# Performance work log

Measured on AMD Instinct MI355X. Metric: run time of the kernel, lower is better.

The kernel has to match this reference:

```python
import jax, jax.numpy as jnp
import numpy as np

D_MODEL = 1024
NUM_HEADS = 16
D_FF = 4096
B = 4
S = 1024
EPS = 1e-5


def _dense_params(key, fan_in, fan_out):
    kw, kb = jax.random.split(key)
    lim = (6.0 / (fan_in + fan_out)) ** 0.5
    w = jax.random.uniform(kw, (fan_in, fan_out), jnp.float32, -lim, lim)
    b = jnp.zeros((fan_out,), jnp.float32)
    return w, b


def setup_inputs() -> dict:
    key = jax.random.key(0)
    ks = jax.random.split(key, 20)
    inp = {
        "x": jax.random.normal(ks[0], (B, S, D_MODEL), jnp.float32),
        "enc_outputs": jax.random.normal(ks[1], (B, S, D_MODEL), jnp.float32),
        "dec_pad_mask": jnp.zeros((B, 1, S, S), jnp.float32),
        "dec_subseq_mask": jnp.zeros((B, 1, S, S), jnp.float32),
    }
    # MHA1 params
    for i, name in enumerate(["wq1", "wk1", "wv1", "wo1"]):
        w, b = _dense_params(ks[2 + i], D_MODEL, D_MODEL)
        inp[name + "_w"], inp[name + "_b"] = w, b
    # MHA2 params
    for i, name in enumerate(["wq2", "wk2", "wv2", "wo2"]):
        w, b = _dense_params(ks[6 + i], D_MODEL, D_MODEL)
        inp[name + "_w"], inp[name + "_b"] = w, b
    # FFN params
    inp["ffn1_w"], inp["ffn1_b"] = _dense_params(ks[10], D_MODEL, D_FF)
    inp["ffn2_w"], inp["ffn2_b"] = _dense_params(ks[11], D_FF, D_MODEL)
    # LayerNorm params
    for i in (1, 2, 3):
        inp[f"ln{i}_g"] = jnp.ones((D_MODEL,), jnp.float32)
        inp[f"ln{i}_b"] = jnp.zeros((D_MODEL,), jnp.float32)
    return inp


def _layernorm(x, g, b):
    mu = jnp.mean(x, axis=-1, keepdims=True)
    var = jnp.mean(jnp.square(x - mu), axis=-1, keepdims=True)
    return (x - mu) * jax.lax.rsqrt(var + EPS) * g + b


def _mha(q_in, k_in, v_in, mask, wq_w, wq_b, wk_w, wk_b, wv_w, wv_b, wo_w, wo_b):
    Bq, Sq, D = q_in.shape
    Sk = k_in.shape[1]
    H = NUM_HEADS
    d = D // H
    # project then split heads: (B, H, S, d)
    q = (q_in @ wq_w + wq_b).reshape(Bq, Sq, H, d).transpose(0, 2, 1, 3)
    k = (k_in @ wk_w + wk_b).reshape(Bq, Sk, H, d).transpose(0, 2, 1, 3)
    v = (v_in @ wv_w + wv_b).reshape(Bq, Sk, H, d).transpose(0, 2, 1, 3)
    logits = jnp.einsum("bhqd,bhkd->bhqk", q, k) / jnp.sqrt(jnp.float32(d))
    if mask is not None:
        logits = logits + mask[:, :, :, :logits.shape[-1]]
    weights = jax.nn.softmax(logits, axis=-1)  # (B, H, Sq, Sk)
    attn = jnp.einsum("bhqk,bhkd->bhqd", weights, v)
    attn = attn.transpose(0, 2, 1, 3).reshape(Bq, Sq, D)
    out = attn @ wo_w + wo_b
    return out, weights


def reference(x, enc_outputs, dec_pad_mask, dec_subseq_mask,
              wq1_w, wq1_b, wk1_w, wk1_b, wv1_w, wv1_b, wo1_w, wo1_b,
              wq2_w, wq2_b, wk2_w, wk2_b, wv2_w, wv2_b, wo2_w, wo2_b,
              ffn1_w, ffn1_b, ffn2_w, ffn2_b,
              ln1_g, ln1_b, ln2_g, ln2_b, ln3_g, ln3_b):
    # self-attention (dropout is identity at inference)
    mha1, attn_w1 = _mha(x, x, x, dec_subseq_mask,
                         wq1_w, wq1_b, wk1_w, wk1_b, wv1_w, wv1_b, wo1_w, wo1_b)
    out1 = _layernorm(mha1 + x, ln1_g, ln1_b)
    # cross-attention
    mha2, attn_w2 = _mha(out1, enc_outputs, enc_outputs, dec_pad_mask,
                         wq2_w, wq2_b, wk2_w, wk2_b, wv2_w, wv2_b, wo2_w, wo2_b)
    out2 = _layernorm(mha2 + out1, ln2_g, ln2_b)
    # FFN
    ffn = jax.nn.relu(out2 @ ffn1_w + ffn1_b) @ ffn2_w + ffn2_b
    out3 = _layernorm(ffn + out2, ln3_g, ln3_b)
    return out3, attn_w1, attn_w2
```

## Files before the change

kernel.cpp:

```cpp
#include <hip/hip_runtime.h>

typedef unsigned short u16;
typedef unsigned int u32;
typedef unsigned long long u64;
typedef __bf16 bf16x8 __attribute__((ext_vector_type(8)));
typedef float f32x4 __attribute__((ext_vector_type(4)));

#define AS1 __attribute__((address_space(1)))
#define AS3 __attribute__((address_space(3)))

__device__ __forceinline__ float bf2f(u32 v) {
    u32 u = v << 16;
    float f;
    __builtin_memcpy(&f, &u, 4);
    return f;
}
__device__ __forceinline__ u16 f2bf(float f) {
    u32 u;
    __builtin_memcpy(&u, &f, 4);
    u32 r = u + 0x7FFFu + ((u >> 16) & 1u);
    return (u16)(r >> 16);
}

template <int BM, int BN, bool RELU, bool SCORES, bool AF32>
__global__ __launch_bounds__(256) void gemm_bt(
    const void* __restrict__ Av, const u16* __restrict__ Bt,
    const float* __restrict__ bias, void* __restrict__ Cv,
    int lda, int ldb, int ldc, int K,
    long Aob, long Aoh, long Bob, long Boh, long Cob, long Coh,
    int batchH, const float* __restrict__ mask, float scale)
{
    const int tid = threadIdx.x;
    const int z = blockIdx.z;
    const int bb = z / batchH, hh = z % batchH;
    const u16*   A16 = AF32 ? nullptr : ((const u16*)Av + (size_t)bb * Aob + (size_t)hh * Aoh);
    const float* A32 = AF32 ? ((const float*)Av + (size_t)bb * Aob + (size_t)hh * Aoh) : nullptr;
    Bt += (size_t)bb * Bob + (size_t)hh * Boh;
    u16*   C16 = SCORES ? nullptr : ((u16*)Cv + (size_t)bb * Cob + (size_t)hh * Coh);
    float* C32 = SCORES ? ((float*)Cv + (size_t)bb * Cob + (size_t)hh * Coh) : nullptr;
    const float* maskp = SCORES ? (mask + ((size_t)bb << 20)) : nullptr;

    const int m0 = blockIdx.y * BM;
    const int n0 = blockIdx.x * BN;

    __shared__ bf16x8 As[AF32 ? BM * 8 : BM * 4];
    __shared__ bf16x8 Bs[BN * 4];

    constexpr int TM = (BN == 128) ? 4 : 2;
    constexpr int TN = 4;
    const int wave = tid >> 6, lane = tid & 63;
    const int wr = (BN == 128) ? (wave >> 1) : wave;
    const int wc = (BN == 128) ? (wave & 1) : 0;
    const int row_base = wr * (TM * 16);
    const int col_base = wc * 64;
    const int quad = lane >> 4, l16 = lane & 15;

    f32x4 acc[TM][TN] = {};

    for (int k0 = 0; k0 < K; k0 += 32) {
        if (AF32) {
#pragma unroll
            for (int i = 0; i < (BM * 8) / 256; ++i) {
                int s = tid + i * 256;
                int row = s >> 3;
                int gq = (s & 7) ^ (row & 7);
                const float* gp = A32 + (size_t)(m0 + row) * lda + k0 + gq * 4;
                __builtin_amdgcn_global_load_lds((AS1 const void*)gp, (AS3 void*)&As[s], 16, 0, 0);
            }
        } else {
#pragma unroll
            for (int i = 0; i < (BM * 4) / 256; ++i) {
                int s = tid + i * 256;
                int row = s >> 2;
                int gq = (s & 3) ^ ((s >> 3) & 3);
                const u16* gp = A16 + (size_t)(m0 + row) * lda + k0 + gq * 8;
                __builtin_amdgcn_global_load_lds((AS1 const void*)gp, (AS3 void*)&As[s], 16, 0, 0);
            }
        }
#pragma unroll
        for (int i = 0; i < (BN * 4) / 256; ++i) {
            int s = tid + i * 256;
            int row = s >> 2;
            int gq = (s & 3) ^ ((s >> 3) & 3);
            const u16* gp = Bt + (size_t)(n0 + row) * ldb + k0 + gq * 8;
            __builtin_amdgcn_global_load_lds((AS1 const void*)gp, (AS3 void*)&Bs[s], 16, 0, 0);
        }
        __syncthreads();

        bf16x8 af[TM], bfr[TN];
#pragma unroll
        for (int ri = 0; ri < TM; ++ri) {
            int r = row_base + ri * 16 + l16;
            if (AF32) {
                const f32x4* Asf = (const f32x4*)As;
                int rx = r & 7;
                f32x4 a0 = Asf[r * 8 + ((2 * quad) ^ rx)];
                f32x4 a1 = Asf[r * 8 + ((2 * quad + 1) ^ rx)];
                union { bf16x8 v; u16 u[8]; } cc;
                cc.u[0] = f2bf(a0[0]); cc.u[1] = f2bf(a0[1]);
                cc.u[2] = f2bf(a0[2]); cc.u[3] = f2bf(a0[3]);
                cc.u[4] = f2bf(a1[0]); cc.u[5] = f2bf(a1[1]);
                cc.u[6] = f2bf(a1[2]); cc.u[7] = f2bf(a1[3]);
                af[ri] = cc.v;
            } else {
                af[ri] = As[r * 4 + (quad ^ ((r >> 1) & 3))];
            }
        }
#pragma unroll
        for (int cj = 0; cj < TN; ++cj) {
            int c = col_base + cj * 16 + l16;
            bfr[cj] = Bs[c * 4 + (quad ^ ((c >> 1) & 3))];
        }
#pragma unroll
        for (int ri = 0; ri < TM; ++ri)
#pragma unroll
            for (int cj = 0; cj < TN; ++cj)
                acc[ri][cj] = __builtin_amdgcn_mfma_f32_16x16x32_bf16(af[ri], bfr[cj], acc[ri][cj], 0, 0, 0);
        __syncthreads();
    }

#pragma unroll
    for (int ri = 0; ri < TM; ++ri) {
#pragma unroll
        for (int cj = 0; cj < TN; ++cj) {
            const int col = n0 + col_base + cj * 16 + l16;
            const float bv = (!SCORES && bias) ? bias[col] : 0.0f;
#pragma unroll
            for (int r = 0; r < 4; ++r) {
                const int row = m0 + row_base + ri * 16 + quad * 4 + r;
                float v = acc[ri][cj][r];
                if (SCORES) {
                    C32[(size_t)row * ldc + col] = v * scale + maskp[((size_t)row << 10) + col];
                } else {
                    v += bv;
                    if (RELU) v = fmaxf(v, 0.0f);
                    C16[(size_t)row * ldc + col] = f2bf(v);
                }
            }
        }
    }
}

__global__ void transpose_cvt(const float* __restrict__ src, u16* __restrict__ dst, int R, int C)
{
    __shared__ u16 t[32][33];
    const int c0 = blockIdx.x << 5, r0 = blockIdx.y << 5;
    const int tx = threadIdx.x, ty = threadIdx.y;
#pragma unroll
    for (int i = 0; i < 4; ++i) {
        int r = r0 + ty * 4 + i;
        t[ty * 4 + i][tx] = f2bf(src[(size_t)r * C + c0 + tx]);
    }
    __syncthreads();
#pragma unroll
    for (int i = 0; i < 4; ++i) {
        int c = c0 + ty * 4 + i;
        dst[(size_t)c * R + r0 + tx] = t[tx][ty * 4 + i];
    }
}

__global__ __launch_bounds__(256) void cvt4(const float* __restrict__ src, u16* __restrict__ dst)
{
    size_t i = (size_t)blockIdx.x * 256 + threadIdx.x;
    f32x4 v = ((const f32x4*)src)[i];
    u64 o = (u64)f2bf(v[0]) | ((u64)f2bf(v[1]) << 16) | ((u64)f2bf(v[2]) << 32) | ((u64)f2bf(v[3]) << 48);
    ((u64*)dst)[i] = o;
}

__global__ void transpose_v(const u16* __restrict__ v, u16* __restrict__ vt)
{
    __shared__ u16 t[32][33];
    const int z = blockIdx.z, b = z >> 4, h = z & 15;
    const int s0 = blockIdx.x << 5, d0 = blockIdx.y << 5;
    const int tx = threadIdx.x, ty = threadIdx.y;
    const u16* src = v + ((size_t)b << 20) + h * 64;
#pragma unroll
    for (int i = 0; i < 4; ++i) {
        int s = s0 + ty * 4 + i;
        t[ty * 4 + i][tx] = src[((size_t)s << 10) + d0 + tx];
    }
    __syncthreads();
    u16* dst = vt + ((size_t)z << 16);
#pragma unroll
    for (int i = 0; i < 4; ++i) {
        int d = d0 + ty * 4 + i;
        dst[((size_t)d << 10) + s0 + tx] = t[tx][ty * 4 + i];
    }
}

__global__ __launch_bounds__(256) void softmax_rows_f32(float* __restrict__ data)
{
    float* p = data + ((size_t)blockIdx.x << 10);
    const int t = threadIdx.x;
    f32x4 v = ((const f32x4*)p)[t];
    float mx = fmaxf(fmaxf(v[0], v[1]), fmaxf(v[2], v[3]));
#pragma unroll
    for (int off = 32; off > 0; off >>= 1) mx = fmaxf(mx, __shfl_xor(mx, off));
    __shared__ float sred[4];
    const int wave = t >> 6, lane = t & 63;
    if (lane == 0) sred[wave] = mx;
    __syncthreads();
    mx = fmaxf(fmaxf(sred[0], sred[1]), fmaxf(sred[2], sred[3]));
    __syncthreads();
    float e0 = __expf(v[0] - mx), e1 = __expf(v[1] - mx);
    float e2 = __expf(v[2] - mx), e3 = __expf(v[3] - mx);
    float s = e0 + e1 + e2 + e3;
#pragma unroll
    for (int off = 32; off > 0; off >>= 1) s += __shfl_xor(s, off);
    if (lane == 0) sred[wave] = s;
    __syncthreads();
    const float inv = 1.0f / (sred[0] + sred[1] + sred[2] + sred[3]);
    f32x4 o;
    o[0] = e0 * inv; o[1] = e1 * inv; o[2] = e2 * inv; o[3] = e3 * inv;
    ((f32x4*)p)[t] = o;
}

template <bool B_F32>
__global__ __launch_bounds__(256) void add_ln(
    const u16* __restrict__ a, const void* __restrict__ bvp,
    const float* __restrict__ g, const float* __restrict__ be,
    u16* __restrict__ out, float* __restrict__ outf)
{
    const size_t row = blockIdx.x;
    const int t = threadIdx.x;
    uint2 va = ((const uint2*)(a + (row << 10)))[t];
    float f0 = bf2f(va.x & 0xffffu), f1 = bf2f(va.x >> 16);
    float f2 = bf2f(va.y & 0xffffu), f3 = bf2f(va.y >> 16);
    if (B_F32) {
        f32x4 vb = ((const f32x4*)((const float*)bvp + (row << 10)))[t];
        f0 += vb[0]; f1 += vb[1]; f2 += vb[2]; f3 += vb[3];
    } else {
        uint2 vb = ((const uint2*)((const u16*)bvp + (row << 10)))[t];
        f0 += bf2f(vb.x & 0xffffu); f1 += bf2f(vb.x >> 16);
        f2 += bf2f(vb.y & 0xffffu); f3 += bf2f(vb.y >> 16);
    }
    float s = f0 + f1 + f2 + f3;
    float q = f0 * f0 + f1 * f1 + f2 * f2 + f3 * f3;
#pragma unroll
    for (int off = 32; off > 0; off >>= 1) {
        s += __shfl_xor(s, off);
        q += __shfl_xor(q, off);
    }
    __shared__ float rs[4], rq[4];
    const int wave = t >> 6, lane = t & 63;
    if (lane == 0) { rs[wave] = s; rq[wave] = q; }
    __syncthreads();
    s = rs[0] + rs[1] + rs[2] + rs[3];
    q = rq[0] + rq[1] + rq[2] + rq[3];
    const float mean = s * (1.0f / 1024.0f);
    const float var = q * (1.0f / 1024.0f) - mean * mean;
    const float rstd = rsqrtf(var + 1e-5f);
    f32x4 vg = ((const f32x4*)g)[t];
    f32x4 ve = ((const f32x4*)be)[t];
    float r0 = (f0 - mean) * rstd * vg[0] + ve[0];
    float r1 = (f1 - mean) * rstd * vg[1] + ve[1];
    float r2 = (f2 - mean) * rstd * vg[2] + ve[2];
    float r3 = (f3 - mean) * rstd * vg[3] + ve[3];
    if (out) {
        u32 o0 = (u32)f2bf(r0) | ((u32)f2bf(r1) << 16);
        u32 o1 = (u32)f2bf(r2) | ((u32)f2bf(r3) << 16);
        ((uint2*)(out + (row << 10)))[t] = make_uint2(o0, o1);
    }
    if (outf) {
        f32x4 o; o[0] = r0; o[1] = r1; o[2] = r2; o[3] = r3;
        ((f32x4*)(outf + (row << 10)))[t] = o;
    }
}

extern "C" void kernel_launch(void* const* d_in, const int* in_sizes, int n_in,
                              void* d_out, int out_size, void* d_ws, size_t ws_size,
                              hipStream_t stream)
{
    const float* X    = (const float*)d_in[0];
    const float* ENC  = (const float*)d_in[1];
    const float* MPAD = (const float*)d_in[2];
    const float* MSUB = (const float*)d_in[3];
    const float* Wq1 = (const float*)d_in[4],  *bq1 = (const float*)d_in[5];
    const float* Wk1 = (const float*)d_in[6],  *bk1 = (const float*)d_in[7];
    const float* Wv1 = (const float*)d_in[8],  *bv1 = (const float*)d_in[9];
    const float* Wo1 = (const float*)d_in[10], *bo1 = (const float*)d_in[11];
    const float* Wq2 = (const float*)d_in[12], *bq2 = (const float*)d_in[13];
    const float* Wk2 = (const float*)d_in[14], *bk2 = (const float*)d_in[15];
    const float* Wv2 = (const float*)d_in[16], *bv2 = (const float*)d_in[17];
    const float* Wo2 = (const float*)d_in[18], *bo2 = (const float*)d_in[19];
    const float* Wf1 = (const float*)d_in[20], *bf1 = (const float*)d_in[21];
    const float* Wf2 = (const float*)d_in[22], *bf2v = (const float*)d_in[23];
    const float* g1 = (const float*)d_in[24], *be1 = (const float*)d_in[25];
    const float* g2 = (const float*)d_in[26], *be2 = (const float*)d_in[27];
    const float* g3 = (const float*)d_in[28], *be3 = (const float*)d_in[29];

    float* OUT3 = (float*)d_out;
    float* AW1  = OUT3 + 4194304;
    float* AW2  = AW1 + 67108864;

    u16* ws = (u16*)d_ws;
    const size_t M1 = 1048576;
    u16* WTq1 = ws + 0 * M1, *WTk1 = ws + 1 * M1, *WTv1 = ws + 2 * M1, *WTo1 = ws + 3 * M1;
    u16* WTq2 = ws + 4 * M1, *WTk2 = ws + 5 * M1, *WTv2 = ws + 6 * M1, *WTo2 = ws + 7 * M1;
    u16* WTF1 = ws + 8 * M1;
    u16* WTF2 = ws + 12 * M1;
    u16* Xbf  = ws + 16 * M1;
    u16* ENCb = ws + 20 * M1;
    u16* Qb = ws + 24 * M1, *Kb = ws + 28 * M1, *Vb = ws + 32 * M1, *VT = ws + 36 * M1;
    u16* Hb = Qb;
    u16* ATT = ws + 40 * M1, *TMP = ws + 44 * M1, *O1 = ws + 48 * M1, *O2 = ws + 52 * M1;

    const dim3 tb(32, 8);
    cvt4<<<4096, 256, 0, stream>>>(X, Xbf);
    cvt4<<<4096, 256, 0, stream>>>(ENC, ENCb);
    transpose_cvt<<<dim3(32, 32), tb, 0, stream>>>(Wq1, WTq1, 1024, 1024);
    transpose_cvt<<<dim3(32, 32), tb, 0, stream>>>(Wk1, WTk1, 1024, 1024);
    transpose_cvt<<<dim3(32, 32), tb, 0, stream>>>(Wv1, WTv1, 1024, 1024);
    transpose_cvt<<<dim3(32, 32), tb, 0, stream>>>(Wo1, WTo1, 1024, 1024);
    transpose_cvt<<<dim3(32, 32), tb, 0, stream>>>(Wq2, WTq2, 1024, 1024);
    transpose_cvt<<<dim3(32, 32), tb, 0, stream>>>(Wk2, WTk2, 1024, 1024);
    transpose_cvt<<<dim3(32, 32), tb, 0, stream>>>(Wv2, WTv2, 1024, 1024);
    transpose_cvt<<<dim3(32, 32), tb, 0, stream>>>(Wo2, WTo2, 1024, 1024);
    transpose_cvt<<<dim3(128, 32), tb, 0, stream>>>(Wf1, WTF1, 1024, 4096);
    transpose_cvt<<<dim3(32, 128), tb, 0, stream>>>(Wf2, WTF2, 4096, 1024);

    gemm_bt<128, 128, false, false, false><<<dim3(8, 32, 1), 256, 0, stream>>>(
        Xbf, WTq1, bq1, Qb, 1024, 1024, 1024, 1024, 0, 0, 0, 0, 0, 0, 1, nullptr, 0.f);
    gemm_bt<128, 128, false, false, false><<<dim3(8, 32, 1), 256, 0, stream>>>(
        Xbf, WTk1, bk1, Kb, 1024, 1024, 1024, 1024, 0, 0, 0, 0, 0, 0, 1, nullptr, 0.f);
    gemm_bt<128, 128, false, false, false><<<dim3(8, 32, 1), 256, 0, stream>>>(
        Xbf, WTv1, bv1, Vb, 1024, 1024, 1024, 1024, 0, 0, 0, 0, 0, 0, 1, nullptr, 0.f);
    transpose_v<<<dim3(32, 2, 64), tb, 0, stream>>>(Vb, VT);
    gemm_bt<128, 128, false, true, false><<<dim3(8, 8, 64), 256, 0, stream>>>(
        Qb, Kb, nullptr, AW1, 1024, 1024, 1024, 64,
        1048576, 64, 1048576, 64, 16777216, 1048576, 16, MSUB, 0.125f);
    softmax_rows_f32<<<65536, 256, 0, stream>>>(AW1);
    gemm_bt<128, 64, false, false, true><<<dim3(1, 8, 64), 256, 0, stream>>>(
        AW1, VT, nullptr, ATT, 1024, 1024, 1024, 1024,
        16777216, 1048576, 1048576, 65536, 1048576, 64, 16, nullptr, 0.f);
    gemm_bt<128, 128, false, false, false><<<dim3(8, 32, 1), 256, 0, stream>>>(
        ATT, WTo1, bo1, TMP, 1024, 1024, 1024, 1024, 0, 0, 0, 0, 0, 0, 1, nullptr, 0.f);
    add_ln<true><<<4096, 256, 0, stream>>>(TMP, X, g1, be1, O1, nullptr);

    gemm_bt<128, 128, false, false, false><<<dim3(8, 32, 1), 256, 0, stream>>>(
        O1, WTq2, bq2, Qb, 1024, 1024, 1024, 1024, 0, 0, 0, 0, 0, 0, 1, nullptr, 0.f);
    gemm_bt<128, 128, false, false, false><<<dim3(8, 32, 1), 256, 0, stream>>>(
        ENCb, WTk2, bk2, Kb, 1024, 1024, 1024, 1024, 0, 0, 0, 0, 0, 0, 1, nullptr, 0.f);
    gemm_bt<128, 128, false, false, false><<<dim3(8, 32, 1), 256, 0, stream>>>(
        ENCb, WTv2, bv2, Vb, 1024, 1024, 1024, 1024, 0, 0, 0, 0, 0, 0, 1, nullptr, 0.f);
    transpose_v<<<dim3(32, 2, 64), tb, 0, stream>>>(Vb, VT);
    gemm_bt<128, 128, false, true, false><<<dim3(8, 8, 64), 256, 0, stream>>>(
        Qb, Kb, nullptr, AW2, 1024, 1024, 1024, 64,
        1048576, 64, 1048576, 64, 16777216, 1048576, 16, MPAD, 0.125f);
    softmax_rows_f32<<<65536, 256, 0, stream>>>(AW2);
    gemm_bt<128, 64, false, false, true><<<dim3(1, 8, 64), 256, 0, stream>>>(
        AW2, VT, nullptr, ATT, 1024, 1024, 1024, 1024,
        16777216, 1048576, 1048576, 65536, 1048576, 64, 16, nullptr, 0.f);
    gemm_bt<128, 128, false, false, false><<<dim3(8, 32, 1), 256, 0, stream>>>(
        ATT, WTo2, bo2, TMP, 1024, 1024, 1024, 1024, 0, 0, 0, 0, 0, 0, 1, nullptr, 0.f);
    add_ln<false><<<4096, 256, 0, stream>>>(TMP, O1, g2, be2, O2, nullptr);

    gemm_bt<128, 128, true, false, false><<<dim3(32, 32, 1), 256, 0, stream>>>(
        O2, WTF1, bf1, Hb, 1024, 1024, 4096, 1024, 0, 0, 0, 0, 0, 0, 1, nullptr, 0.f);
    gemm_bt<128, 128, false, false, false><<<dim3(8, 32, 1), 256, 0, stream>>>(
        Hb, WTF2, bf2v, TMP, 4096, 4096, 1024, 4096, 0, 0, 0, 0, 0, 0, 1, nullptr, 0.f);
    add_ln<false><<<4096, 256, 0, stream>>>(TMP, O2, g3, be3, nullptr, OUT3);
}
```

Measured before the change: 1.523 ms.

## Fuse attention scores, softmax and PV into one kernel; merge QKV projections

Replaces the separate scores GEMM, row softmax, and f32-A PV GEMM with a fused two-pass attention kernel. The first pass computes the running row max and sum; the second recomputes scores, writes the normalized weights once, and multiplies by V from LDS. Q/K/V projections (and cross-attention K/V) are merged into single wider GEMMs with concatenated weights and biases, and the output projections use narrower tiles for more blocks. This removes the fp32 score round-trips through global memory, at the cost of computing QK^T twice.

```diff
diff --git a/kernel.cpp b/kernel.cpp
--- a/kernel.cpp
+++ b/kernel.cpp
@@ -22,28 +22,17 @@
     return (u16)(r >> 16);
 }
 
-template <int BM, int BN, bool RELU, bool SCORES, bool AF32>
+template <int BM, int BN, bool RELU>
 __global__ __launch_bounds__(256) void gemm_bt(
-    const void* __restrict__ Av, const u16* __restrict__ Bt,
-    const float* __restrict__ bias, void* __restrict__ Cv,
-    int lda, int ldb, int ldc, int K,
-    long Aob, long Aoh, long Bob, long Boh, long Cob, long Coh,
-    int batchH, const float* __restrict__ mask, float scale)
+    const u16* __restrict__ A, const u16* __restrict__ Bt,
+    const float* __restrict__ bias, u16* __restrict__ C,
+    int lda, int ldb, int ldc, int K)
 {
     const int tid = threadIdx.x;
-    const int z = blockIdx.z;
-    const int bb = z / batchH, hh = z % batchH;
-    const u16*   A16 = AF32 ? nullptr : ((const u16*)Av + (size_t)bb * Aob + (size_t)hh * Aoh);
-    const float* A32 = AF32 ? ((const float*)Av + (size_t)bb * Aob + (size_t)hh * Aoh) : nullptr;
-    Bt += (size_t)bb * Bob + (size_t)hh * Boh;
-    u16*   C16 = SCORES ? nullptr : ((u16*)Cv + (size_t)bb * Cob + (size_t)hh * Coh);
-    float* C32 = SCORES ? ((float*)Cv + (size_t)bb * Cob + (size_t)hh * Coh) : nullptr;
-    const float* maskp = SCORES ? (mask + ((size_t)bb << 20)) : nullptr;
-
     const int m0 = blockIdx.y * BM;
     const int n0 = blockIdx.x * BN;
 
-    __shared__ bf16x8 As[AF32 ? BM * 8 : BM * 4];
+    __shared__ bf16x8 As[BM * 4];
     __shared__ bf16x8 Bs[BN * 4];
 
     constexpr int TM = (BN == 128) ? 4 : 2;
@@ -58,24 +47,13 @@
     f32x4 acc[TM][TN] = {};
 
     for (int k0 = 0; k0 < K; k0 += 32) {
-        if (AF32) {
-#pragma unroll
-            for (int i = 0; i < (BM * 8) / 256; ++i) {
-                int s = tid + i * 256;
-                int row = s >> 3;
-                int gq = (s & 7) ^ (row & 7);
-                const float* gp = A32 + (size_t)(m0 + row) * lda + k0 + gq * 4;
-                __builtin_amdgcn_global_load_lds((AS1 const void*)gp, (AS3 void*)&As[s], 16, 0, 0);
-            }
-        } else {
-#pragma unroll
-            for (int i = 0; i < (BM * 4) / 256; ++i) {
-                int s = tid + i * 256;
-                int row = s >> 2;
-                int gq = (s & 3) ^ ((s >> 3) & 3);
-                const u16* gp = A16 + (size_t)(m0 + row) * lda + k0 + gq * 8;
-                __builtin_amdgcn_global_load_lds((AS1 const void*)gp, (AS3 void*)&As[s], 16, 0, 0);
-            }
+#pragma unroll
+        for (int i = 0; i < (BM * 4) / 256; ++i) {
+            int s = tid + i * 256;
+            int row = s >> 2;
+            int gq = (s & 3) ^ ((s >> 3) & 3);
+            const u16* gp = A + (size_t)(m0 + row) * lda + k0 + gq * 8;
+            __builtin_amdgcn_global_load_lds((AS1 const void*)gp, (AS3 void*)&As[s], 16, 0, 0);
         }
 #pragma unroll
         for (int i = 0; i < (BN * 4) / 256; ++i) {
@@ -91,20 +69,7 @@
 #pragma unroll
         for (int ri = 0; ri < TM; ++ri) {
             int r = row_base + ri * 16 + l16;
-            if (AF32) {
-                const f32x4* Asf = (const f32x4*)As;
-                int rx = r & 7;
-                f32x4 a0 = Asf[r * 8 + ((2 * quad) ^ rx)];
-                f32x4 a1 = Asf[r * 8 + ((2 * quad + 1) ^ rx)];
-                union { bf16x8 v; u16 u[8]; } cc;
-                cc.u[0] = f2bf(a0[0]); cc.u[1] = f2bf(a0[1]);
-                cc.u[2] = f2bf(a0[2]); cc.u[3] = f2bf(a0[3]);
-                cc.u[4] = f2bf(a1[0]); cc.u[5] = f2bf(a1[1]);
-                cc.u[6] = f2bf(a1[2]); cc.u[7] = f2bf(a1[3]);
-                af[ri] = cc.v;
-            } else {
-                af[ri] = As[r * 4 + (quad ^ ((r >> 1) & 3))];
-            }
+            af[ri] = As[r * 4 + (quad ^ ((r >> 1) & 3))];
         }
 #pragma unroll
         for (int cj = 0; cj < TN; ++cj) {
@@ -124,21 +89,190 @@
 #pragma unroll
         for (int cj = 0; cj < TN; ++cj) {
             const int col = n0 + col_base + cj * 16 + l16;
-            const float bv = (!SCORES && bias) ? bias[col] : 0.0f;
+            const float bv = bias ? bias[col] : 0.0f;
 #pragma unroll
             for (int r = 0; r < 4; ++r) {
                 const int row = m0 + row_base + ri * 16 + quad * 4 + r;
-                float v = acc[ri][cj][r];
-                if (SCORES) {
-                    C32[(size_t)row * ldc + col] = v * scale + maskp[((size_t)row << 10) + col];
-                } else {
-                    v += bv;
-                    if (RELU) v = fmaxf(v, 0.0f);
-                    C16[(size_t)row * ldc + col] = f2bf(v);
+                float v = acc[ri][cj][r] + bv;
+                if (RELU) v = fmaxf(v, 0.0f);
+                C[(size_t)row * ldc + col] = f2bf(v);
+            }
+        }
+    }
+}
+
+__global__ __launch_bounds__(256, 2) void attn_fused(
+    const u16* __restrict__ Qp, const u16* __restrict__ Kp, const u16* __restrict__ VTp,
+    const float* __restrict__ mask, float* __restrict__ AW, u16* __restrict__ ATT,
+    int ldq, int ldk)
+{
+    const int tid = threadIdx.x;
+    const int wave = tid >> 6, lane = tid & 63, quad = lane >> 4, l16 = lane & 15;
+    const int z = blockIdx.y, b = z >> 4, h = z & 15;
+    const int m0 = blockIdx.x << 7;
+
+    const u16* Q = Qp + (size_t)(b * 1024 + m0) * ldq + h * 64;
+    const u16* K = Kp + (size_t)(b * 1024) * ldk + h * 64;
+    const u16* VT = VTp + ((size_t)z << 16);
+    const float* Mq = mask + ((size_t)b << 20) + ((size_t)m0 << 10);
+    float* AWp = AW + ((size_t)z << 20) + ((size_t)m0 << 10);
+    u16* Op = ATT + ((size_t)(b * 1024 + m0) << 10) + h * 64;
+
+    __shared__ bf16x8 Qs[128 * 8];
+    __shared__ bf16x8 Ks[128 * 8];
+    __shared__ u64 Ps[4][1024];
+
+    bf16x8* Vs = Qs;
+
+#pragma unroll
+    for (int i = 0; i < 4; ++i) {
+        int s = tid + i * 256;
+        int row = s >> 3, ch = s & 7;
+        const u16* gp = Q + (size_t)row * ldq + ((ch ^ (row & 7)) << 3);
+        __builtin_amdgcn_global_load_lds((AS1 const void*)gp, (AS3 void*)&Qs[s], 16, 0, 0);
+    }
+    __syncthreads();
+
+    bf16x8 bq[2][2];
+#pragma unroll
+    for (int qj = 0; qj < 2; ++qj) {
+        int q = wave * 32 + qj * 16 + l16;
+#pragma unroll
+        for (int dstep = 0; dstep < 2; ++dstep)
+            bq[qj][dstep] = Qs[q * 8 + ((dstep * 4 + quad) ^ (q & 7))];
+    }
+
+    float m_run[2] = {-1e30f, -1e30f};
+    float l_run[2] = {0.0f, 0.0f};
+
+    for (int kt = 0; kt < 8; ++kt) {
+#pragma unroll
+        for (int i = 0; i < 4; ++i) {
+            int s = tid + i * 256;
+            int row = s >> 3, ch = s & 7;
+            const u16* gp = K + (size_t)(kt * 128 + row) * ldk + ((ch ^ (row & 7)) << 3);
+            __builtin_amdgcn_global_load_lds((AS1 const void*)gp, (AS3 void*)&Ks[s], 16, 0, 0);
+        }
+        __syncthreads();
+
+        f32x4 acc[8][2] = {};
+#pragma unroll
+        for (int ki = 0; ki < 8; ++ki) {
+            int key = ki * 16 + l16;
+            bf16x8 ka0 = Ks[key * 8 + (quad ^ (key & 7))];
+            bf16x8 ka1 = Ks[key * 8 + ((4 + quad) ^ (key & 7))];
+#pragma unroll
+            for (int qj = 0; qj < 2; ++qj) {
+                acc[ki][qj] = __builtin_amdgcn_mfma_f32_16x16x32_bf16(ka0, bq[qj][0], acc[ki][qj], 0, 0, 0);
+                acc[ki][qj] = __builtin_amdgcn_mfma_f32_16x16x32_bf16(ka1, bq[qj][1], acc[ki][qj], 0, 0, 0);
+            }
+        }
+#pragma unroll
+        for (int qj = 0; qj < 2; ++qj) {
+            const float* mrow = Mq + (((size_t)(wave * 32 + qj * 16 + l16)) << 10) + kt * 128 + quad * 4;
+            float mx = -1e30f;
+#pragma unroll
+            for (int ki = 0; ki < 8; ++ki) {
+                f32x4 mk = *(const f32x4*)(mrow + ki * 16);
+#pragma unroll
+                for (int r = 0; r < 4; ++r) {
+                    float s = fmaf(acc[ki][qj][r], 0.125f, mk[r]);
+                    acc[ki][qj][r] = s;
+                    mx = fmaxf(mx, s);
                 }
             }
-        }
-    }
+            mx = fmaxf(mx, __shfl_xor(mx, 16));
+            mx = fmaxf(mx, __shfl_xor(mx, 32));
+            float mnew = fmaxf(m_run[qj], mx);
+            float sum = 0.0f;
+#pragma unroll
+            for (int ki = 0; ki < 8; ++ki)
+#pragma unroll
+                for (int r = 0; r < 4; ++r)
+                    sum += __expf(acc[ki][qj][r] - mnew);
+            sum += __shfl_xor(sum, 16);
+            sum += __shfl_xor(sum, 32);
+            l_run[qj] = l_run[qj] * __expf(m_run[qj] - mnew) + sum;
+            m_run[qj] = mnew;
+        }
+        __syncthreads();
+    }
+
+    const float invl[2] = {1.0f / l_run[0], 1.0f / l_run[1]};
+    u64* Pw = Ps[wave];
+    const bf16x8* Pr = (const bf16x8*)Ps[wave];
+    f32x4 opv[4][2] = {};
+
+    for (int kt = 0; kt < 8; ++kt) {
+#pragma unroll
+        for (int i = 0; i < 4; ++i) {
+            int s = tid + i * 256;
+            int row = s >> 3, ch = s & 7;
+            const u16* gp = K + (size_t)(kt * 128 + row) * ldk + ((ch ^ (row & 7)) << 3);
+            __builtin_amdgcn_global_load_lds((AS1 const void*)gp, (AS3 void*)&Ks[s], 16, 0, 0);
+        }
+#pragma unroll
+        for (int i = 0; i < 4; ++i) {
+            int s = tid + i * 256;
+            int row = s >> 4, ch = s & 15;
+            const u16* gp = VT + ((size_t)row << 10) + kt * 128 + ((ch ^ (row & 15)) << 3);
+            __builtin_amdgcn_global_load_lds((AS1 const void*)gp, (AS3 void*)&Vs[s], 16, 0, 0);
+        }
+        __syncthreads();
+
+#pragma unroll
+        for (int ki = 0; ki < 8; ++ki) {
+            int key = ki * 16 + l16;
+            bf16x8 ka0 = Ks[key * 8 + (quad ^ (key & 7))];
+            bf16x8 ka1 = Ks[key * 8 + ((4 + quad) ^ (key & 7))];
+#pragma unroll
+            for (int qj = 0; qj < 2; ++qj) {
+                f32x4 a = {};
+                a = __builtin_amdgcn_mfma_f32_16x16x32_bf16(ka0, bq[qj][0], a, 0, 0, 0);
+                a = __builtin_amdgcn_mfma_f32_16x16x32_bf16(ka1, bq[qj][1], a, 0, 0, 0);
+                const size_t roff = ((size_t)(wave * 32 + qj * 16 + l16)) << 10;
+                f32x4 mk = *(const f32x4*)(Mq + roff + kt * 128 + ki * 16 + quad * 4);
+                f32x4 p;
+#pragma unroll
+                for (int r = 0; r < 4; ++r)
+                    p[r] = __expf(fmaf(a[r], 0.125f, mk[r]) - m_run[qj]) * invl[qj];
+                *(f32x4*)(AWp + roff + kt * 128 + ki * 16 + quad * 4) = p;
+                u64 pk = (u64)f2bf(p[0]) | ((u64)f2bf(p[1]) << 16)
+                       | ((u64)f2bf(p[2]) << 32) | ((u64)f2bf(p[3]) << 48);
+                int q = qj * 16 + l16;
+                Pw[q * 32 + ((ki * 4 + quad) ^ ((q & 7) << 1))] = pk;
+            }
+        }
+
+#pragma unroll
+        for (int ks = 0; ks < 4; ++ks) {
+            bf16x8 pb[2];
+#pragma unroll
+            for (int qj = 0; qj < 2; ++qj) {
+                int q = qj * 16 + l16;
+                pb[qj] = Pr[q * 16 + ((ks * 4 + quad) ^ (q & 7))];
+            }
+#pragma unroll
+            for (int ds = 0; ds < 4; ++ds) {
+                int d = ds * 16 + l16;
+                bf16x8 va = Vs[d * 16 + ((ks * 4 + quad) ^ (d & 15))];
+                opv[ds][0] = __builtin_amdgcn_mfma_f32_16x16x32_bf16(va, pb[0], opv[ds][0], 0, 0, 0);
+                opv[ds][1] = __builtin_amdgcn_mfma_f32_16x16x32_bf16(va, pb[1], opv[ds][1], 0, 0, 0);
+            }
+        }
+        __syncthreads();
+    }
+
+#pragma unroll
+    for (int ds = 0; ds < 4; ++ds)
+#pragma unroll
+        for (int qj = 0; qj < 2; ++qj) {
+            int q = wave * 32 + qj * 16 + l16;
+            f32x4 v = opv[ds][qj];
+            u64 o = (u64)f2bf(v[0]) | ((u64)f2bf(v[1]) << 16)
+                  | ((u64)f2bf(v[2]) << 32) | ((u64)f2bf(v[3]) << 48);
+            *(u64*)(Op + (((size_t)q) << 10) + ds * 16 + quad * 4) = o;
+        }
 }
 
 __global__ void transpose_cvt(const float* __restrict__ src, u16* __restrict__ dst, int R, int C)
@@ -167,17 +301,17 @@
     ((u64*)dst)[i] = o;
 }
 
-__global__ void transpose_v(const u16* __restrict__ v, u16* __restrict__ vt)
+__global__ void transpose_v(const u16* __restrict__ v, u16* __restrict__ vt, int ld)
 {
     __shared__ u16 t[32][33];
     const int z = blockIdx.z, b = z >> 4, h = z & 15;
     const int s0 = blockIdx.x << 5, d0 = blockIdx.y << 5;
     const int tx = threadIdx.x, ty = threadIdx.y;
-    const u16* src = v + ((size_t)b << 20) + h * 64;
+    const u16* src = v + (size_t)(b << 10) * ld + h * 64;
 #pragma unroll
     for (int i = 0; i < 4; ++i) {
         int s = s0 + ty * 4 + i;
-        t[ty * 4 + i][tx] = src[((size_t)s << 10) + d0 + tx];
+        t[ty * 4 + i][tx] = src[(size_t)s * ld + d0 + tx];
     }
     __syncthreads();
     u16* dst = vt + ((size_t)z << 16);
@@ -188,31 +322,12 @@
     }
 }
 
-__global__ __launch_bounds__(256) void softmax_rows_f32(float* __restrict__ data)
-{
-    float* p = data + ((size_t)blockIdx.x << 10);
-    const int t = threadIdx.x;
-    f32x4 v = ((const f32x4*)p)[t];
-    float mx = fmaxf(fmaxf(v[0], v[1]), fmaxf(v[2], v[3]));
-#pragma unroll
-    for (int off = 32; off > 0; off >>= 1) mx = fmaxf(mx, __shfl_xor(mx, off));
-    __shared__ float sred[4];
-    const int wave = t >> 6, lane = t & 63;
-    if (lane == 0) sred[wave] = mx;
-    __syncthreads();
-    mx = fmaxf(fmaxf(sred[0], sred[1]), fmaxf(sred[2], sred[3]));
-    __syncthreads();
-    float e0 = __expf(v[0] - mx), e1 = __expf(v[1] - mx);
-    float e2 = __expf(v[2] - mx), e3 = __expf(v[3] - mx);
-    float s = e0 + e1 + e2 + e3;
-#pragma unroll
-    for (int off = 32; off > 0; off >>= 1) s += __shfl_xor(s, off);
-    if (lane == 0) sred[wave] = s;
-    __syncthreads();
-    const float inv = 1.0f / (sred[0] + sred[1] + sred[2] + sred[3]);
-    f32x4 o;
-    o[0] = e0 * inv; o[1] = e1 * inv; o[2] = e2 * inv; o[3] = e3 * inv;
-    ((f32x4*)p)[t] = o;
+__global__ void concat3(const float* __restrict__ a, const float* __restrict__ b,
+                        const float* __restrict__ c, float* __restrict__ o, int n)
+{
+    int i = blockIdx.x * 256 + threadIdx.x;
+    float v = (i < n) ? a[i] : (i < 2 * n) ? b[i - n] : c[i - 2 * n];
+    o[i] = v;
 }
 
 template <bool B_F32>
@@ -295,69 +410,66 @@
 
     u16* ws = (u16*)d_ws;
     const size_t M1 = 1048576;
-    u16* WTq1 = ws + 0 * M1, *WTk1 = ws + 1 * M1, *WTv1 = ws + 2 * M1, *WTo1 = ws + 3 * M1;
-    u16* WTq2 = ws + 4 * M1, *WTk2 = ws + 5 * M1, *WTv2 = ws + 6 * M1, *WTo2 = ws + 7 * M1;
+    u16* WTqkv1 = ws + 0 * M1;
+    u16* WTo1 = ws + 3 * M1;
+    u16* WTkv2 = ws + 4 * M1;
+    u16* WTq2 = ws + 6 * M1;
+    u16* WTo2 = ws + 7 * M1;
     u16* WTF1 = ws + 8 * M1;
     u16* WTF2 = ws + 12 * M1;
     u16* Xbf  = ws + 16 * M1;
     u16* ENCb = ws + 20 * M1;
-    u16* Qb = ws + 24 * M1, *Kb = ws + 28 * M1, *Vb = ws + 32 * M1, *VT = ws + 36 * M1;
-    u16* Hb = Qb;
-    u16* ATT = ws + 40 * M1, *TMP = ws + 44 * M1, *O1 = ws + 48 * M1, *O2 = ws + 52 * M1;
+    u16* QKV1 = ws + 24 * M1;
+    u16* Q2b  = ws + 24 * M1;
+    u16* KV2  = ws + 28 * M1;
+    u16* Hb   = ws + 24 * M1;
+    u16* VT   = ws + 36 * M1;
+    u16* ATT  = ws + 40 * M1;
+    u16* TMP  = ws + 44 * M1;
+    u16* O1   = ws + 48 * M1;
+    u16* O2   = ws + 52 * M1;
+    float* BQKV1 = (float*)(ws + 56 * M1);
+    float* BKV2  = BQKV1 + 3072;
 
     const dim3 tb(32, 8);
     cvt4<<<4096, 256, 0, stream>>>(X, Xbf);
     cvt4<<<4096, 256, 0, stream>>>(ENC, ENCb);
-    transpose_cvt<<<dim3(32, 32), tb, 0, stream>>>(Wq1, WTq1, 1024, 1024);
-    transpose_cvt<<<dim3(32, 32), tb, 0, stream>>>(Wk1, WTk1, 1024, 1024);
-    transpose_cvt<<<dim3(32, 32), tb, 0, stream>>>(Wv1, WTv1, 1024, 1024);
+    transpose_cvt<<<dim3(32, 32), tb, 0, stream>>>(Wq1, WTqkv1, 1024, 1024);
+    transpose_cvt<<<dim3(32, 32), tb, 0, stream>>>(Wk1, WTqkv1 + 1 * M1, 1024, 1024);
+    transpose_cvt<<<dim3(32, 32), tb, 0, stream>>>(Wv1, WTqkv1 + 2 * M1, 1024, 1024);
     transpose_cvt<<<dim3(32, 32), tb, 0, stream>>>(Wo1, WTo1, 1024, 1024);
+    transpose_cvt<<<dim3(32, 32), tb, 0, stream>>>(Wk2, WTkv2, 1024, 1024);
+    transpose_cvt<<<dim3(32, 32), tb, 0, stream>>>(Wv2, WTkv2 + 1 * M1, 1024, 1024);
     transpose_cvt<<<dim3(32, 32), tb, 0, stream>>>(Wq2, WTq2, 1024, 1024);
-    transpose_cvt<<<dim3(32, 32), tb, 0, stream>>>(Wk2, WTk2, 1024, 1024);
-    transpose_cvt<<<dim3(32, 32), tb, 0, stream>>>(Wv2, WTv2, 1024, 1024);
     transpose_cvt<<<dim3(32, 32), tb, 0, stream>>>(Wo2, WTo2, 1024, 1024);
     transpose_cvt<<<dim3(128, 32), tb, 0, stream>>>(Wf1, WTF1, 1024, 4096);
     transpose_cvt<<<dim3(32, 128), tb, 0, stream>>>(Wf2, WTF2, 4096, 1024);
-
-    gemm_bt<128, 128, false, false, false><<<dim3(8, 32, 1), 256, 0, stream>>>(
-        Xbf, WTq1, bq1, Qb, 1024, 1024, 1024, 1024, 0, 0, 0, 0, 0, 0, 1, nullptr, 0.f);
-    gemm_bt<128, 128, false, false, false><<<dim3(8, 32, 1), 256, 0, stream>>>(
-        Xbf, WTk1, bk1, Kb, 1024, 1024, 1024, 1024, 0, 0, 0, 0, 0, 0, 1, nullptr, 0.f);
-    gemm_bt<128, 128, false, false, false><<<dim3(8, 32, 1), 256, 0, stream>>>(
-        Xbf, WTv1, bv1, Vb, 1024, 1024, 1024, 1024, 0, 0, 0, 0, 0, 0, 1, nullptr, 0.f);
-    transpose_v<<<dim3(32, 2, 64), tb, 0, stream>>>(Vb, VT);
-    gemm_bt<128, 128, false, true, false><<<dim3(8, 8, 64), 256, 0, stream>>>(
-        Qb, Kb, nullptr, AW1, 1024, 1024, 1024, 64,
-        1048576, 64, 1048576, 64, 16777216, 1048576, 16, MSUB, 0.125f);
-    softmax_rows_f32<<<65536, 256, 0, stream>>>(AW1);
-    gemm_bt<128, 64, false, false, true><<<dim3(1, 8, 64), 256, 0, stream>>>(
-        AW1, VT, nullptr, ATT, 1024, 1024, 1024, 1024,
-        16777216, 1048576, 1048576, 65536, 1048576, 64, 16, nullptr, 0.f);
-    gemm_bt<128, 128, false, false, false><<<dim3(8, 32, 1), 256, 0, stream>>>(
-        ATT, WTo1, bo1, TMP, 1024, 1024, 1024, 1024, 0, 0, 0, 0, 0, 0, 1, nullptr, 0.f);
+    concat3<<<12, 256, 0, stream>>>(bq1, bk1, bv1, BQKV1, 1024);
+    concat3<<<8, 256, 0, stream>>>(bk2, bv2, bv2, BKV2, 1024);
+
+    gemm_bt<128, 128, false><<<dim3(24, 32), 256, 0, stream>>>(
+        Xbf, WTqkv1, BQKV1, QKV1, 1024, 1024, 3072, 1024);
+    transpose_v<<<dim3(32, 2, 64), tb, 0, stream>>>(QKV1 + 2048, VT, 3072);
+    attn_fused<<<dim3(8, 64), 256, 0, stream>>>(
+        QKV1, QKV1 + 1024, VT, MSUB, AW1, ATT, 3072, 3072);
+    gemm_bt<128, 64, false><<<dim3(16, 32), 256, 0, stream>>>(
+        ATT, WTo1, bo1, TMP, 1024, 1024, 1024, 1024);
     add_ln<true><<<4096, 256, 0, stream>>>(TMP, X, g1, be1, O1, nullptr);
 
-    gemm_bt<128, 128, false, false, false><<<dim3(8, 32, 1), 256, 0, stream>>>(
-        O1, WTq2, bq2, Qb, 1024, 1024, 1024, 1024, 0, 0, 0, 0, 0, 0, 1, nullptr, 0.f);
-    gemm_bt<128, 128, false, false, false><<<dim3(8, 32, 1), 256, 0, stream>>>(
-        ENCb, WTk2, bk2, Kb, 1024, 1024, 1024, 1024, 0, 0, 0, 0, 0, 0, 1, nullptr, 0.f);
-    gemm_bt<128, 128, false, false, false><<<dim3(8, 32, 1), 256, 0, stream>>>(
-        ENCb, WTv2, bv2, Vb, 1024, 1024, 1024, 1024, 0, 0, 0, 0, 0, 0, 1, nullptr, 0.f);
-    transpose_v<<<dim3(32, 2, 64), tb, 0, stream>>>(Vb, VT);
-    gemm_bt<128, 128, false, true, false><<<dim3(8, 8, 64), 256, 0, stream>>>(
-        Qb, Kb, nullptr, AW2, 1024, 1024, 1024, 64,
-        1048576, 64, 1048576, 64, 16777216, 1048576, 16, MPAD, 0.125f);
-    softmax_rows_f32<<<65536, 256, 0, stream>>>(AW2);
-    gemm_bt<128, 64, false, false, true><<<dim3(1, 8, 64), 256, 0, stream>>>(
-        AW2, VT, nullptr, ATT, 1024, 1024, 1024, 1024,
-        16777216, 1048576, 1048576, 65536, 1048576, 64, 16, nullptr, 0.f);
-    gemm_bt<128, 128, false, false, false><<<dim3(8, 32, 1), 256, 0, stream>>>(
-        ATT, WTo2, bo2, TMP, 1024, 1024, 1024, 1024, 0, 0, 0, 0, 0, 0, 1, nullptr, 0.f);
+    gemm_bt<128, 64, false><<<dim3(16, 32), 256, 0, stream>>>(
+        O1, WTq2, bq2, Q2b, 1024, 1024, 1024, 1024);
+    gemm_bt<128, 128, false><<<dim3(16, 32), 256, 0, stream>>>(
+        ENCb, WTkv2, BKV2, KV2, 1024, 1024, 2048, 1024);
+    transpose_v<<<dim3(32, 2, 64), tb, 0, stream>>>(KV2 + 1024, VT, 2048);
+    attn_fused<<<dim3(8, 64), 256, 0, stream>>>(
+        Q2b, KV2, VT, MPAD, AW2, ATT, 1024, 2048);
+    gemm_bt<128, 64, false><<<dim3(16, 32), 256, 0, stream>>>(
+        ATT, WTo2, bo2, TMP, 1024, 1024, 1024, 1024);
     add_ln<false><<<4096, 256, 0, stream>>>(TMP, O1, g2, be2, O2, nullptr);
 
-    gemm_bt<128, 128, true, false, false><<<dim3(32, 32, 1), 256, 0, stream>>>(
-        O2, WTF1, bf1, Hb, 1024, 1024, 4096, 1024, 0, 0, 0, 0, 0, 0, 1, nullptr, 0.f);
-    gemm_bt<128, 128, false, false, false><<<dim3(8, 32, 1), 256, 0, stream>>>(
-        Hb, WTF2, bf2v, TMP, 4096, 4096, 1024, 4096, 0, 0, 0, 0, 0, 0, 1, nullptr, 0.f);
+    gemm_bt<128, 128, true><<<dim3(32, 32), 256, 0, stream>>>(
+        O2, WTF1, bf1, Hb, 1024, 1024, 4096, 1024);
+    gemm_bt<128, 128, false><<<dim3(8, 32), 256, 0, stream>>>(
+        Hb, WTF2, bf2v, TMP, 4096, 4096, 1024, 4096);
     add_ln<false><<<4096, 256, 0, stream>>>(TMP, O2, g3, be3, nullptr, OUT3);
 }
```

Measured after the change: 1.297 ms. -14.8%, faster.
